# Performance work log

Hardware: AMD Instinct MI355X
Metric: run time of the kernel (lower is better)

## Reference

```python
import jax, jax.numpy as jnp
import numpy as np
from functools import partial

ALPHA, TAG, L, B = 128, 64, 50, 4096
EMB, CTX, ATT, FREQ, OUTLEN = 40, 20, 100, 60, 50
START = 1  # Alphabet.start_integer


def _sinusoid(n, d):
    # RNN_Absolute_Position: standard sinusoidal positional code, d freqs
    pos = jnp.arange(n, dtype=jnp.float32)[:, None]
    i = jnp.arange(d // 2, dtype=jnp.float32)[None, :]
    ang = pos / jnp.power(10000.0, 2.0 * i / d)
    return jnp.concatenate([jnp.sin(ang), jnp.cos(ang)], axis=-1)  # [n, d]


def _shift_back(x, k):   # value at t-k (zeros for t<k); OffsetWindows(-k)
    return jnp.pad(x, ((k, 0), (0, 0), (0, 0)))[: x.shape[0]]


def _shift_fwd(x, k):    # value at t+k (zeros past end); OffsetWindows(+k)
    return jnp.pad(x, ((0, k), (0, 0), (0, 0)))[k:]


def setup_inputs() -> dict:
    key = jax.random.key(0)
    ks = jax.random.split(key, 16)

    def lin(k, din, dout):
        k1, k2 = jax.random.split(k)
        s = 1.0 / np.sqrt(din)
        return (jax.random.uniform(k1, (din, dout), minval=-s, maxval=s),
                jax.random.uniform(k2, (dout,), minval=-s, maxval=s))

    W_ce, b_ce = lin(ks[0], EMB, CTX)                      # encoder context_embedder
    W_b4, b_b4 = lin(ks[1], 2 * CTX, CTX)                  # before_context (2 prev steps)
    W_aft, b_aft = lin(ks[2], CTX, CTX)                    # after_context (1 next step)
    W_all, b_all = lin(ks[3], 2 * CTX, CTX)                # all_context
    W_re, b_re = lin(ks[4], ALPHA, CTX)                    # decoder context_reembedder
    W_bc, b_bc = lin(ks[5], CTX, CTX)                      # decoder before_context (1 prev)
    W_q, b_q = lin(ks[6], FREQ + CTX + ALPHA + TAG, ATT)   # attention query net
    W_k, b_k = lin(ks[7], FREQ + CTX + EMB, ATT)           # attention key net
    ff_in = (CTX + EMB) + (CTX + ALPHA) + (CTX + ALPHA + TAG)
    W_ff, b_ff = lin(ks[8], ff_in, ALPHA)                  # decoder ff
    emb_table = jax.random.normal(ks[9], (ALPHA, EMB))
    lemma = jax.random.randint(ks[10], (L, B), 0, ALPHA)
    tags = jax.random.uniform(ks[11], (B, TAG))
    return dict(lemma=lemma, tags=tags, emb_table=emb_table,
                W_ce=W_ce, b_ce=b_ce, W_b4=W_b4, b_b4=b_b4,
                W_aft=W_aft, b_aft=b_aft, W_all=W_all, b_all=b_all,
                W_re=W_re, b_re=b_re, W_bc=W_bc, b_bc=b_bc,
                W_q=W_q, b_q=b_q, W_k=W_k, b_k=b_k, W_ff=W_ff, b_ff=b_ff)


def reference(lemma, tags, emb_table, W_ce, b_ce, W_b4, b_b4, W_aft, b_aft,
              W_all, b_all, W_re, b_re, W_bc, b_bc, W_q, b_q, W_k, b_k,
              W_ff, b_ff):
    Lc, Bc = lemma.shape
    sig = jax.nn.sigmoid

    # ---- LetterContextEncoder ----
    emb = emb_table[lemma]                                  # [L,B,EMB]
    ce = emb @ W_ce + b_ce                                  # [L,B,CTX]
    b4 = sig(jnp.concatenate([_shift_back(ce, 2), _shift_back(ce, 1)], -1) @ W_b4 + b_b4)
    aft = sig(_shift_fwd(ce, 1) @ W_aft + b_aft)
    ctxt = sig(jnp.concatenate([b4, aft], -1) @ W_all + b_all)  # [L,B,CTX]

    # ---- DumberDecoder (vectorized over batch) ----
    input_stack = jnp.concatenate([ctxt, emb], -1)          # [L,B,CTX+EMB]
    abs_pos = _sinusoid(OUTLEN, FREQ)                       # [OUTLEN,FREQ]
    pos_b = jnp.broadcast_to(abs_pos[:Lc, None, :], (Lc, Bc, FREQ))
    pos_stack = jnp.concatenate([pos_b, input_stack], -1)   # [L,B,120]
    K = sig(pos_stack @ W_k + b_k)                          # [L,B,ATT] precomputed keys
    V = input_stack

    # probs[0] is one-hot start token
    probs0 = jnp.zeros((Bc, ALPHA)).at[:, START].set(1.0)
    r0 = jnp.zeros((Bc, CTX))                               # reembed of probs[-1] == 0
    zeros_oa = jnp.zeros((Bc, CTX + ALPHA))                 # output_attention_results
    T = min(OUTLEN, Lc)

    def step(carry, i):
        probs_prev, r_pp = carry                            # probs[i-1], reembed(probs[i-2])
        ctx = sig(r_pp @ W_bc + b_bc)                       # output_context[i-1]
        pos_i = jnp.broadcast_to(abs_pos[i][None, :], (Bc, FREQ))
        q_in = jnp.concatenate([pos_i, ctx, probs_prev, tags], -1)
        q = sig(q_in @ W_q + b_q)                           # [B,ATT]
        scores = jnp.einsum('ba,lba->bl', q, K)
        attn = jax.nn.softmax(scores, axis=-1)
        in_attn = jnp.einsum('bl,lbd->bd', attn, V)         # [B,CTX+EMB]
        x = jnp.concatenate([in_attn, zeros_oa, ctx, probs_prev, tags], -1)
        p = jax.nn.softmax(sig(x @ W_ff + b_ff), axis=-1)   # [B,ALPHA]
        r_new = sig(probs_prev @ W_re + b_re)
        return (p, r_new), p

    _, ps = jax.lax.scan(step, (probs0, r0), jnp.arange(1, T))
    return jnp.concatenate([probs0[None], ps], axis=0)      # [T,B,ALPHA]
```

## Files before the change

### kernel.cpp

```cpp
#include <hip/hip_runtime.h>

using fp16 = _Float16;
typedef fp16 f16x4 __attribute__((ext_vector_type(4)));
typedef fp16 f16x8 __attribute__((ext_vector_type(8)));
typedef float f32x4 __attribute__((ext_vector_type(4)));

#define DEVI __device__ __forceinline__

constexpr int LL = 50;
constexpr int BB = 4096;
constexpr int ALPHA = 128;
constexpr int CTX = 20;
constexpr int ATT = 100;
constexpr int EPB = 16;

constexpr int FQ_OFF  = 0;
constexpr int FF_OFF  = 17920;
constexpr int FR_OFF  = 46592;
constexpr int FB_OFF  = 50688;
constexpr int FTQ_OFF = 51712;
constexpr int FTF_OFF = 58880;
constexpr int FRAG_TOT= 67072;

constexpr size_t WS_FRAG = 0;
constexpr size_t WS_PQ   = 134144;
constexpr size_t WS_PK   = 156544;
constexpr size_t WS_TBL  = 178944;
constexpr int    TBL_CE  = 0;
constexpr int    TBL_EM  = 2560;
constexpr int    TBL_WK  = 7680;
constexpr int    TBL_N   = 15744;
constexpr size_t WS_K    = 210432;
constexpr size_t WS_V    = WS_K + (size_t)BB*5200*2;

constexpr int XQS = 168, XFS = 232, QBS = 104, SCS = 136, TQS = 104, ATS = 56;
constexpr int OFF_XQ = 0;
constexpr int OFF_XF = 5376;
constexpr int OFF_RP = 12800;
constexpr int OFF_QB = 14080;
constexpr int OFF_SC = 17408;
constexpr int OFF_AT = 21760;
constexpr int OFF_TQ = 23552;
constexpr int OFF_TF = 26880;
constexpr int OFF_CX = 30976;
constexpr int OFF_BB = 31616;
constexpr int OFF_V  = 31776;
constexpr int SM_TOT = 131616;

DEVI float rcpf(float x) { return __builtin_amdgcn_rcpf(x); }
DEVI float sigm(float x) { return rcpf(1.0f + __expf(-x)); }

DEVI f32x4 mfma16(f16x8 a, f16x8 b, f32x4 c) {
  return __builtin_amdgcn_mfma_f32_16x16x32_f16(a, b, c, 0, 0, 0);
}
DEVI float dot8f(f16x8 a, f16x8 b, float acc) {
  acc = __builtin_amdgcn_fdot2(__builtin_shufflevector(a,a,0,1), __builtin_shufflevector(b,b,0,1), acc, false);
  acc = __builtin_amdgcn_fdot2(__builtin_shufflevector(a,a,2,3), __builtin_shufflevector(b,b,2,3), acc, false);
  acc = __builtin_amdgcn_fdot2(__builtin_shufflevector(a,a,4,5), __builtin_shufflevector(b,b,4,5), acc, false);
  acc = __builtin_amdgcn_fdot2(__builtin_shufflevector(a,a,6,7), __builtin_shufflevector(b,b,6,7), acc, false);
  return acc;
}
DEVI float dot4f(f16x4 a, f16x4 b, float acc) {
  acc = __builtin_amdgcn_fdot2(__builtin_shufflevector(a,a,0,1), __builtin_shufflevector(b,b,0,1), acc, false);
  acc = __builtin_amdgcn_fdot2(__builtin_shufflevector(a,a,2,3), __builtin_shufflevector(b,b,2,3), acc, false);
  return acc;
}

#define DPP_STEP(OP, CTRL)                                                        \
  { int t_ = __builtin_amdgcn_update_dpp(0, __builtin_bit_cast(int, v), CTRL, 0xF, 0xF, true); \
    v = OP(v, __builtin_bit_cast(float, t_)); }
DEVI float addf(float a, float b) { return a + b; }
DEVI float redmax64(float v) {
  DPP_STEP(fmaxf, 0x111) DPP_STEP(fmaxf, 0x112) DPP_STEP(fmaxf, 0x114)
  DPP_STEP(fmaxf, 0x118) DPP_STEP(fmaxf, 0x142) DPP_STEP(fmaxf, 0x143)
  return __builtin_bit_cast(float, __builtin_amdgcn_readlane(__builtin_bit_cast(int, v), 63));
}
DEVI float redsum64(float v) {
  DPP_STEP(addf, 0x111) DPP_STEP(addf, 0x112) DPP_STEP(addf, 0x114)
  DPP_STEP(addf, 0x118) DPP_STEP(addf, 0x142) DPP_STEP(addf, 0x143)
  return __builtin_bit_cast(float, __builtin_amdgcn_readlane(__builtin_bit_cast(int, v), 63));
}

DEVI void lbar() { asm volatile("s_waitcnt lgkmcnt(0)\ns_barrier" ::: "memory"); }

__global__ void dt_setup(const float* __restrict__ embT, const float* __restrict__ Wce,
                         const float* __restrict__ bce,
                         const float* __restrict__ Wq, const float* __restrict__ bq,
                         const float* __restrict__ Wk, const float* __restrict__ bk,
                         const float* __restrict__ Wff, const float* __restrict__ Wre,
                         const float* __restrict__ Wbc, char* __restrict__ ws) {
  __shared__ float ap[LL*60];
  const int tid = threadIdx.x, bid = blockIdx.x;
  if (bid <= 1) {
    for (int i = tid; i < LL*30; i += 256) {
      int p = i / 30, k = i % 30;
      float freq = powf(10000.f, 2.0f*(float)k/60.0f);
      float ang = (float)p / freq;
      ap[p*60 + k]      = sinf(ang);
      ap[p*60 + 30 + k] = cosf(ang);
    }
    __syncthreads();
    const float* W = (bid == 0) ? Wq : Wk;
    const float* bi = (bid == 0) ? bq : bk;
    float* dst = (float*)(ws + (bid == 0 ? WS_PQ : WS_PK));
    for (int i = tid; i < LL*112; i += 256) {
      int r = i / 112, j = i % 112;
      float a = 0.f;
      if (j < ATT) {
        a = bi[j];
        for (int f = 0; f < 60; ++f) a += ap[r*60 + f]*W[f*ATT + j];
      }
      dst[i] = a;
    }
  } else if (bid == 2) {
    fp16* tbl = (fp16*)(ws + WS_TBL);
    for (int i = tid; i < ALPHA*CTX; i += 256) {
      int r = i / CTX, o = i % CTX;
      float a = bce[o];
      for (int e = 0; e < 40; ++e) a += embT[r*40 + e]*Wce[e*CTX + o];
      tbl[TBL_CE + i] = (fp16)a;
    }
    for (int i = tid; i < ALPHA*40; i += 256) tbl[TBL_EM + i] = (fp16)embT[i];
  } else if (bid == 3) {
    fp16* tbl = (fp16*)(ws + WS_TBL);
    for (int i = tid; i < 112*72; i += 256) {
      int a = i / 72, c = i % 72;
      float v = 0.f;
      if (a < ATT) {
        if (c < 20)      v = Wk[(60 + c)*ATT + a];
        else if (c < 60) v = Wk[(80 + (c-20))*ATT + a];
      }
      tbl[TBL_WK + i] = (fp16)v;
    }
  } else {
    fp16* pw = (fp16*)(ws + WS_FRAG);
    for (int gi = (bid-4)*256 + tid; gi < FRAG_TOT; gi += 28*256) {
      int t = gi, img, base, KT;
      if      (t < FF_OFF)  { img = 0; base = t - FQ_OFF;  KT = 5; }
      else if (t < FR_OFF)  { img = 1; base = t - FF_OFF;  KT = 7; }
      else if (t < FB_OFF)  { img = 2; base = t - FR_OFF;  KT = 4; }
      else if (t < FTQ_OFF) { img = 3; base = t - FB_OFF;  KT = 1; }
      else if (t < FTF_OFF) { img = 4; base = t - FTQ_OFF; KT = 2; }
      else                  { img = 5; base = t - FTF_OFF; KT = 2; }
      int j = base & 7, lane = (base >> 3) & 63, frag = base >> 9;
      int nt = frag / KT, kt = frag % KT;
      int k = kt*32 + ((lane >> 4) << 3) + j;
      int n = nt*16 + (lane & 15);
      float v = 0.f;
      if (img == 0) {
        if (n < ATT) {
          if (k < 128)      v = Wq[(80 + k)*ATT + n];
          else if (k < 148) v = Wq[(60 + (k - 128))*ATT + n];
        }
      } else if (img == 1) {
        if (k < 128)      v = Wff[(228 + k)*ALPHA + n];
        else if (k < 188) v = Wff[(k - 128)*ALPHA + n];
        else if (k < 208) v = Wff[(208 + (k - 188))*ALPHA + n];
      } else if (img == 2) {
        if (k < 128 && n < CTX) v = Wre[k*CTX + n];
      } else if (img == 3) {
        if (k < CTX && n < CTX) v = Wbc[k*CTX + n];
      } else if (img == 4) {
        if (n < ATT && k < 64)  v = Wq[(208 + k)*ATT + n];
      } else {
        if (k < 64)             v = Wff[(356 + k)*ALPHA + n];
      }
      pw[gi] = (fp16)v;
    }
  }
}

__global__ void dt_encode(const int* __restrict__ lemma,
    const float* __restrict__ Wb4, const float* __restrict__ bb4,
    const float* __restrict__ Waft, const float* __restrict__ baft,
    const float* __restrict__ Wall, const float* __restrict__ ball,
    char* __restrict__ ws) {
  __shared__ fp16 wkl[112*72];
  __shared__ float wb4[800], wa[400], wl[800];
  __shared__ float cel[LL*CTX], b4l[LL*CTX], afl[LL*CTX];
  __shared__ fp16 xin[LL*72];
  __shared__ float bi4[CTX], biA[CTX], biL[CTX];
  __shared__ int lem[52];
  const int b = blockIdx.x, tid = threadIdx.x;
  const fp16* ceg = (const fp16*)(ws + WS_TBL) + TBL_CE;
  const fp16* emg = (const fp16*)(ws + WS_TBL) + TBL_EM;

  { const uint4* s = (const uint4*)((const fp16*)(ws + WS_TBL) + TBL_WK);
    uint4* d = (uint4*)wkl;
    for (int i = tid; i < 112*72*2/16; i += 256) d[i] = s[i]; }
  { const float4* s = (const float4*)Wb4; float4* d = (float4*)wb4;
    for (int i = tid; i < 200; i += 256) d[i] = s[i]; }
  { const float4* s = (const float4*)Waft; float4* d = (float4*)wa;
    for (int i = tid; i < 100; i += 256) d[i] = s[i]; }
  { const float4* s = (const float4*)Wall; float4* d = (float4*)wl;
    for (int i = tid; i < 200; i += 256) d[i] = s[i]; }
  if (tid < CTX) { bi4[tid] = bb4[tid]; biA[tid] = baft[tid]; biL[tid] = ball[tid]; }
  if (tid < LL) lem[tid] = lemma[tid*BB + b];
  __syncthreads();

  for (int i = tid; i < LL*CTX; i += 256)
    cel[i] = (float)ceg[lem[i/CTX]*CTX + (i % CTX)];
  __syncthreads();

  for (int i = tid; i < LL*CTX; i += 256) {
    int l = i / CTX, o = i % CTX;
    float a = bi4[o];
    for (int c = 0; c < CTX; ++c) {
      float c2 = (l >= 2) ? cel[(l-2)*CTX + c] : 0.f;
      float c1 = (l >= 1) ? cel[(l-1)*CTX + c] : 0.f;
      a += c2*wb4[c*CTX + o] + c1*wb4[(CTX+c)*CTX + o];
    }
    b4l[i] = sigm(a);
    float af = biA[o];
    if (l < LL-1)
      for (int c = 0; c < CTX; ++c) af += cel[(l+1)*CTX + c]*wa[c*CTX + o];
    afl[i] = sigm(af);
  }
  __syncthreads();

  for (int i = tid; i < LL*CTX; i += 256) {
    int l = i / CTX, o = i % CTX;
    float a = biL[o];
    for (int c = 0; c < CTX; ++c)
      a += b4l[l*CTX + c]*wl[c*CTX + o] + afl[l*CTX + c]*wl[(CTX+c)*CTX + o];
    xin[l*72 + o] = (fp16)sigm(a);
  }
  for (int i = tid; i < LL*40; i += 256) {
    int l = i / 40, d = i % 40;
    xin[l*72 + 20 + d] = emg[lem[l]*40 + d];
  }
  for (int i = tid; i < LL*12; i += 256) {
    int l = i / 12, c = i % 12;
    xin[l*72 + 60 + c] = (fp16)0.f;
  }
  __syncthreads();

  const float* pkg = (const float*)(ws + WS_PK);
  fp16* Kw = (fp16*)(ws + WS_K) + (size_t)b*5200;
  for (int i = tid; i < 5200; i += 256) {
    int l = i / 104, a = i % 104;
    fp16 v = (fp16)0.f;
    if (a < ATT) {
      float acc = pkg[l*112 + a];
      const fp16* x = xin + l*72;
      const fp16* wv = wkl + a*72;
      #pragma unroll
      for (int k = 0; k < 9; ++k)
        acc = dot8f(*(const f16x8*)(x + 8*k), *(const f16x8*)(wv + 8*k), acc);
      v = (fp16)sigm(acc);
    }
    Kw[i] = v;
  }
  fp16* Vw = (fp16*)(ws + WS_V) + (size_t)b*3120;
  for (int i = tid; i < 3120; i += 256) {
    int d = i / 52, l = i % 52;
    Vw[i] = (l < LL) ? xin[l*72 + d] : (fp16)0.f;
  }
}

__global__ __launch_bounds__(1024)
void dt_decoder(const char* __restrict__ ws, const float* __restrict__ tags,
                const float* __restrict__ b_re, const float* __restrict__ b_bc,
                const float* __restrict__ bff, float* __restrict__ out) {
  extern __shared__ char sm[];
  fp16* xq   = (fp16*)(sm + OFF_XQ);
  fp16* xf   = (fp16*)(sm + OFF_XF);
  fp16* rp   = (fp16*)(sm + OFF_RP);
  fp16* qb   = (fp16*)(sm + OFF_QB);
  fp16* sc   = (fp16*)(sm + OFF_SC);
  fp16* atb  = (fp16*)(sm + OFF_AT);
  fp16* tagq = (fp16*)(sm + OFF_TQ);
  fp16* tagf = (fp16*)(sm + OFF_TF);
  fp16* ctxs = (fp16*)(sm + OFF_CX);
  float* bbv = (float*)(sm + OFF_BB);
  fp16* Vl   = (fp16*)(sm + OFF_V);
  fp16* tagsl = (fp16*)(sm + OFF_QB);

  const int tid = threadIdx.x, lane = tid & 63, w = tid >> 6;
  const int quad = lane >> 4, col = lane & 15;
  const int koff = quad * 8, r0 = quad * 4;
  const int b0 = blockIdx.x * EPB;
  const int b = b0 + w;

  { uint* z = (uint*)sm;
    for (int j = tid; j < OFF_TQ/4; j += 1024) z[j] = 0; }
  { const uint4* s = (const uint4*)(ws + WS_V + (size_t)b0*6240);
    uint4* d = (uint4*)Vl;
    for (int j = tid; j < EPB*390; j += 1024) d[j] = s[j]; }
  if (tid < CTX) { bbv[tid] = b_re[tid]; bbv[20 + tid] = b_bc[tid]; }
  const float bffr = bff[((w & 7) << 4) + col];
  __syncthreads();

  { int e = tid >> 6, c = tid & 63;
    tagsl[e*72 + c] = (fp16)tags[(size_t)(b0 + e)*64 + c]; }
  if (tid < EPB) { xq[tid*XQS + 1] = (fp16)1.f; xf[tid*XFS + 1] = (fp16)1.f; }
  if (tid < EPB*CTX) {
    int r = tid / CTX, o = tid % CTX;
    float c1 = sigm(b_bc[o]);
    xq[r*XQS + 128 + o] = (fp16)c1;
    xf[r*XFS + 188 + o] = (fp16)c1;
  }
  for (int j = tid; j < EPB*128; j += 1024) {
    int e = j >> 7, o = j & 127;
    out[(size_t)(b0 + e)*ALPHA + o] = (o == 1) ? 1.f : 0.f;
  }
  __syncthreads();

  const fp16* fw = (const fp16*)(ws + WS_FRAG);
  {
    f16x8 a0 = *(const f16x8*)(tagsl + (lane & 15)*72 + koff);
    f16x8 a1 = *(const f16x8*)(tagsl + (lane & 15)*72 + 32 + koff);
    if (w < 7) {
      f16x8 t0 = *(const f16x8*)(fw + FTQ_OFF + (((w*2 + 0) << 6) + lane)*8);
      f16x8 t1 = *(const f16x8*)(fw + FTQ_OFF + (((w*2 + 1) << 6) + lane)*8);
      f32x4 c = {0.f,0.f,0.f,0.f};
      c = mfma16(a0, t0, c); c = mfma16(a1, t1, c);
      const int colg = w*16 + col;
      if (colg < 104) {
        #pragma unroll
        for (int r = 0; r < 4; ++r) tagq[(r0 + r)*TQS + colg] = (fp16)c[r];
      }
    } else if (w >= 8) {
      f16x8 u0 = *(const f16x8*)(fw + FTF_OFF + ((((w-8)*2 + 0) << 6) + lane)*8);
      f16x8 u1 = *(const f16x8*)(fw + FTF_OFF + ((((w-8)*2 + 1) << 6) + lane)*8);
      f32x4 d = {0.f,0.f,0.f,0.f};
      d = mfma16(a0, u0, d); d = mfma16(a1, u1, d);
      const int colg = (w-8)*16 + col;
      #pragma unroll
      for (int r = 0; r < 4; ++r) tagf[(r0 + r)*128 + colg] = (fp16)(d[r] + bffr);
    }
  }

  f16x8 KW[13], wW[10];
  { const int lrow = (lane < LL) ? lane : LL-1;
    const fp16* kg = (const fp16*)(ws + WS_K) + (size_t)b*5200 + lrow*104;
    #pragma unroll
    for (int j = 0; j < 13; ++j) KW[j] = *(const f16x8*)(kg + 8*j); }
  if (w < 7) {
    #pragma unroll
    for (int kt = 0; kt < 5; ++kt)
      wW[kt] = *(const f16x8*)(fw + FQ_OFF + (((w*5 + kt) << 6) + lane)*8);
  } else if (w == 7) {
    #pragma unroll
    for (int j = 0; j < 8; ++j)
      wW[j] = *(const f16x8*)(fw + FR_OFF + ((j << 6) + lane)*8);
    wW[8] = *(const f16x8*)(fw + FB_OFF + ((0 << 6) + lane)*8);
    wW[9] = *(const f16x8*)(fw + FB_OFF + ((1 << 6) + lane)*8);
  } else {
    #pragma unroll
    for (int kt = 0; kt < 7; ++kt)
      wW[kt] = *(const f16x8*)(fw + FF_OFF + ((((w-8)*7 + kt) << 6) + lane)*8);
  }

  const float* posqg = (const float*)(ws + WS_PQ);
  const fp16* xq_a = xq + (lane & 15)*XQS + koff;
  const fp16* xf_a = xf + (lane & 15)*XFS + koff;
  const fp16* rp_a = rp + (lane & 15)*40 + koff;

  __syncthreads();

  float pA = 0.f, pB = 0.f;

  for (int i = 1; i < LL; ++i) {
    if (i > 1) {
      size_t ob = ((size_t)(i-1)*BB + b)*ALPHA;
      out[ob + lane] = pA; out[ob + 64 + lane] = pB;
    }
    if (w < 7) {
      const int colg = w*16 + col;
      float pos = posqg[i*112 + colg];
      f32x4 c0 = {0.f,0.f,0.f,0.f}, c1 = {0.f,0.f,0.f,0.f};
      c0 = mfma16(*(const f16x8*)(xq_a + 0*32), wW[0], c0);
      c1 = mfma16(*(const f16x8*)(xq_a + 1*32), wW[1], c1);
      c0 = mfma16(*(const f16x8*)(xq_a + 2*32), wW[2], c0);
      c1 = mfma16(*(const f16x8*)(xq_a + 3*32), wW[3], c1);
      c0 = mfma16(*(const f16x8*)(xq_a + 4*32), wW[4], c0);
      if (colg < 104) {
        #pragma unroll
        for (int r = 0; r < 4; ++r)
          qb[(r0 + r)*QBS + colg] =
            (fp16)sigm(c0[r] + c1[r] + pos + (float)tagq[(r0 + r)*TQS + colg]);
      }
    } else if (w == 7) {
      f32x4 c0 = {0.f,0.f,0.f,0.f}, c1 = {0.f,0.f,0.f,0.f};
      #pragma unroll
      for (int kt = 0; kt < 4; ++kt) {
        f16x8 a = *(const f16x8*)(xq_a + kt*32);
        c0 = mfma16(a, wW[kt],     c0);
        c1 = mfma16(a, wW[4 + kt], c1);
      }
      const int cA = col, cB = 16 + col;
      #pragma unroll
      for (int r = 0; r < 4; ++r) {
        rp[(r0 + r)*40 + cA] = (fp16)sigm(c0[r] + bbv[cA]);
        if (cB < CTX) rp[(r0 + r)*40 + cB] = (fp16)sigm(c1[r] + bbv[cB]);
      }
      f16x8 ar = *(const f16x8*)rp_a;
      f32x4 d0 = mfma16(ar, wW[8], (f32x4){0.f,0.f,0.f,0.f});
      f32x4 d1 = mfma16(ar, wW[9], (f32x4){0.f,0.f,0.f,0.f});
      #pragma unroll
      for (int r = 0; r < 4; ++r) {
        ctxs[(r0 + r)*20 + cA] = (fp16)sigm(d0[r] + bbv[20 + cA]);
        if (cB < CTX) ctxs[(r0 + r)*20 + cB] = (fp16)sigm(d1[r] + bbv[20 + cB]);
      }
    }
    lbar();

    {
      const fp16* qrow = qb + w*QBS;
      float a0 = 0.f, a1 = 0.f;
      #pragma unroll
      for (int k = 0; k < 12; k += 2) {
        a0 = dot8f(*(const f16x8*)(qrow + 8*k),     KW[k],   a0);
        a1 = dot8f(*(const f16x8*)(qrow + 8*(k+1)), KW[k+1], a1);
      }
      a0 = dot8f(*(const f16x8*)(qrow + 96), KW[12], a0);
      float s = (lane < LL) ? (a0 + a1) : 0.f;
      float m  = redmax64(s);
      float e  = (lane < LL) ? __expf(s - m) : 0.f;
      float su = redsum64(e);
      if (lane < LL) atb[w*ATS + lane] = (fp16)(e * rcpf(su));
      const fp16* ar = atb + w*ATS;
      const fp16* vr = Vl + (w*60 + ((lane < 60) ? lane : 59))*52;
      float v0 = 0.f, v1 = 0.f;
      #pragma unroll
      for (int k = 0; k < 12; k += 2) {
        v0 = dot4f(*(const f16x4*)(ar + 4*k),     *(const f16x4*)(vr + 4*k),     v0);
        v1 = dot4f(*(const f16x4*)(ar + 4*(k+1)), *(const f16x4*)(vr + 4*(k+1)), v1);
      }
      v0 = dot4f(*(const f16x4*)(ar + 48), *(const f16x4*)(vr + 48), v0);
      if (lane < 60) xf[w*XFS + 128 + lane] = (fp16)(v0 + v1);
    }
    lbar();

    if (w >= 8) {
      const int colg = (w-8)*16 + col;
      f32x4 c0 = {0.f,0.f,0.f,0.f}, c1 = {0.f,0.f,0.f,0.f};
      c0 = mfma16(*(const f16x8*)(xf_a + 0*32), wW[0], c0);
      c1 = mfma16(*(const f16x8*)(xf_a + 1*32), wW[1], c1);
      c0 = mfma16(*(const f16x8*)(xf_a + 2*32), wW[2], c0);
      c1 = mfma16(*(const f16x8*)(xf_a + 3*32), wW[3], c1);
      c0 = mfma16(*(const f16x8*)(xf_a + 4*32), wW[4], c0);
      c1 = mfma16(*(const f16x8*)(xf_a + 5*32), wW[5], c1);
      c0 = mfma16(*(const f16x8*)(xf_a + 6*32), wW[6], c0);
      #pragma unroll
      for (int r = 0; r < 4; ++r)
        sc[(r0 + r)*SCS + colg] =
          (fp16)sigm(c0[r] + c1[r] + (float)tagf[(r0 + r)*128 + colg]);
    }
    lbar();

    {
      float v0 = (float)sc[w*SCS + lane], v1 = (float)sc[w*SCS + 64 + lane];
      float m = redmax64(fmaxf(v0, v1));
      float e0 = __expf(v0 - m), e1 = __expf(v1 - m);
      float su = redsum64(e0 + e1);
      float inv = rcpf(su);
      pA = e0 * inv; pB = e1 * inv;
      xq[w*XQS + lane] = (fp16)pA; xq[w*XQS + 64 + lane] = (fp16)pB;
      xf[w*XFS + lane] = (fp16)pA; xf[w*XFS + 64 + lane] = (fp16)pB;
    }
    if (w == 7) {
      int r = lane & 15, cg = (lane >> 4) * 5;
      #pragma unroll
      for (int j = 0; j < 5; ++j) {
        fp16 t = ctxs[r*20 + cg + j];
        xq[r*XQS + 128 + cg + j] = t;
        xf[r*XFS + 188 + cg + j] = t;
      }
    }
    lbar();
  }
  { size_t ob = ((size_t)(LL-1)*BB + b)*ALPHA;
    out[ob + lane] = pA; out[ob + 64 + lane] = pB; }
}

extern "C" void kernel_launch(void* const* d_in, const int* in_sizes, int n_in,
                              void* d_out, int out_size, void* d_ws, size_t ws_size,
                              hipStream_t stream) {
  (void)in_sizes; (void)n_in; (void)out_size; (void)ws_size;
  const int*   lemma = (const int*)  d_in[0];
  const float* tags  = (const float*)d_in[1];
  const float* embT  = (const float*)d_in[2];
  const float* Wce   = (const float*)d_in[3];
  const float* bce   = (const float*)d_in[4];
  const float* Wb4   = (const float*)d_in[5];
  const float* bb4   = (const float*)d_in[6];
  const float* Waft  = (const float*)d_in[7];
  const float* baft  = (const float*)d_in[8];
  const float* Wall  = (const float*)d_in[9];
  const float* ball  = (const float*)d_in[10];
  const float* Wre   = (const float*)d_in[11];
  const float* bre   = (const float*)d_in[12];
  const float* Wbc   = (const float*)d_in[13];
  const float* bbc   = (const float*)d_in[14];
  const float* Wq    = (const float*)d_in[15];
  const float* bq    = (const float*)d_in[16];
  const float* Wk    = (const float*)d_in[17];
  const float* bk    = (const float*)d_in[18];
  const float* Wff   = (const float*)d_in[19];
  const float* bff   = (const float*)d_in[20];
  char* ws = (char*)d_ws;
  float* out = (float*)d_out;

  hipFuncSetAttribute((const void*)dt_decoder,
                      hipFuncAttributeMaxDynamicSharedMemorySize, SM_TOT);

  dt_setup<<<32, 256, 0, stream>>>(embT, Wce, bce, Wq, bq, Wk, bk, Wff, Wre, Wbc, ws);
  dt_encode<<<BB, 256, 0, stream>>>(lemma, Wb4, bb4, Waft, baft, Wall, ball, ws);
  dt_decoder<<<BB/EPB, 1024, SM_TOT, stream>>>(ws, tags, bre, bbc, bff, out);
}
```

Before: 522.0 us.

## Compute attention scores with MFMA and reload weight fragments per step

The per-warp attention score dot products (fdot2 over K rows held in registers) become 16x16x32 MFMA tiles. Each warp holds key fragments for 16-position chunks, and the diagonal entry for its own batch row is extracted through a new shared scratch buffer, with a small dot-product tail for the last 4 attention dims. The per-warp weight fragments (wW) are no longer held in registers. They are reloaded from global/L2 inside every step, which frees registers at the cost of repeated loads. The MFMA computes all 16x16 batch-by-position products but only the diagonal row is used, so most of that work is wasted.

```diff
diff --git a/kernel.cpp b/kernel.cpp
--- a/kernel.cpp
+++ b/kernel.cpp
@@ -34,18 +34,19 @@
 constexpr size_t WS_V    = WS_K + (size_t)BB*5200*2;
 
 constexpr int XQS = 168, XFS = 232, QBS = 104, SCS = 136, TQS = 104, ATS = 56;
-constexpr int OFF_XQ = 0;
-constexpr int OFF_XF = 5376;
-constexpr int OFF_RP = 12800;
-constexpr int OFF_QB = 14080;
-constexpr int OFF_SC = 17408;
-constexpr int OFF_AT = 21760;
-constexpr int OFF_TQ = 23552;
-constexpr int OFF_TF = 26880;
-constexpr int OFF_CX = 30976;
-constexpr int OFF_BB = 31616;
-constexpr int OFF_V  = 31776;
-constexpr int SM_TOT = 131616;
+constexpr int OFF_XQ  = 0;
+constexpr int OFF_XF  = 5376;
+constexpr int OFF_RP  = 12800;
+constexpr int OFF_QB  = 14080;
+constexpr int OFF_SC  = 17408;
+constexpr int OFF_AT  = 21760;
+constexpr int OFF_TQ  = 23552;
+constexpr int OFF_TF  = 26880;
+constexpr int OFF_CX  = 30976;
+constexpr int OFF_BB  = 31616;
+constexpr int OFF_SCW = 31776;
+constexpr int OFF_V   = 35872;
+constexpr int SM_TOT  = 135712;
 
 DEVI float rcpf(float x) { return __builtin_amdgcn_rcpf(x); }
 DEVI float sigm(float x) { return rcpf(1.0f + __expf(-x)); }
@@ -273,6 +274,7 @@
   fp16* tagf = (fp16*)(sm + OFF_TF);
   fp16* ctxs = (fp16*)(sm + OFF_CX);
   float* bbv = (float*)(sm + OFF_BB);
+  float* scw = (float*)(sm + OFF_SCW);
   fp16* Vl   = (fp16*)(sm + OFF_V);
   fp16* tagsl = (fp16*)(sm + OFF_QB);
 
@@ -288,7 +290,6 @@
     uint4* d = (uint4*)Vl;
     for (int j = tid; j < EPB*390; j += 1024) d[j] = s[j]; }
   if (tid < CTX) { bbv[tid] = b_re[tid]; bbv[20 + tid] = b_bc[tid]; }
-  const float bffr = bff[((w & 7) << 4) + col];
   __syncthreads();
 
   { int e = tid >> 6, c = tid & 63;
@@ -308,8 +309,8 @@
 
   const fp16* fw = (const fp16*)(ws + WS_FRAG);
   {
-    f16x8 a0 = *(const f16x8*)(tagsl + (lane & 15)*72 + koff);
-    f16x8 a1 = *(const f16x8*)(tagsl + (lane & 15)*72 + 32 + koff);
+    f16x8 a0 = *(const f16x8*)(tagsl + col*72 + koff);
+    f16x8 a1 = *(const f16x8*)(tagsl + col*72 + 32 + koff);
     if (w < 7) {
       f16x8 t0 = *(const f16x8*)(fw + FTQ_OFF + (((w*2 + 0) << 6) + lane)*8);
       f16x8 t1 = *(const f16x8*)(fw + FTQ_OFF + (((w*2 + 1) << 6) + lane)*8);
@@ -321,6 +322,7 @@
         for (int r = 0; r < 4; ++r) tagq[(r0 + r)*TQS + colg] = (fp16)c[r];
       }
     } else if (w >= 8) {
+      const float bffr = bff[(w-8)*16 + col];
       f16x8 u0 = *(const f16x8*)(fw + FTF_OFF + ((((w-8)*2 + 0) << 6) + lane)*8);
       f16x8 u1 = *(const f16x8*)(fw + FTF_OFF + ((((w-8)*2 + 1) << 6) + lane)*8);
       f32x4 d = {0.f,0.f,0.f,0.f};
@@ -331,31 +333,25 @@
     }
   }
 
-  f16x8 KW[13], wW[10];
-  { const int lrow = (lane < LL) ? lane : LL-1;
-    const fp16* kg = (const fp16*)(ws + WS_K) + (size_t)b*5200 + lrow*104;
+  f16x8 KF[12];
+  f16x4 ktail;
+  { const fp16* kg = (const fp16*)(ws + WS_K) + (size_t)b*5200;
     #pragma unroll
-    for (int j = 0; j < 13; ++j) KW[j] = *(const f16x8*)(kg + 8*j); }
-  if (w < 7) {
-    #pragma unroll
-    for (int kt = 0; kt < 5; ++kt)
-      wW[kt] = *(const f16x8*)(fw + FQ_OFF + (((w*5 + kt) << 6) + lane)*8);
-  } else if (w == 7) {
-    #pragma unroll
-    for (int j = 0; j < 8; ++j)
-      wW[j] = *(const f16x8*)(fw + FR_OFF + ((j << 6) + lane)*8);
-    wW[8] = *(const f16x8*)(fw + FB_OFF + ((0 << 6) + lane)*8);
-    wW[9] = *(const f16x8*)(fw + FB_OFF + ((1 << 6) + lane)*8);
-  } else {
-    #pragma unroll
-    for (int kt = 0; kt < 7; ++kt)
-      wW[kt] = *(const f16x8*)(fw + FF_OFF + ((((w-8)*7 + kt) << 6) + lane)*8);
+    for (int c = 0; c < 3; ++c) {
+      #pragma unroll
+      for (int t = 0; t < 4; ++t) {
+        int pos = t*16 + col; if (pos >= LL) pos = LL-1;
+        KF[c*4 + t] = *(const f16x8*)(kg + pos*104 + c*32 + koff);
+      }
+    }
+    int pl = (lane < LL) ? lane : LL-1;
+    ktail = *(const f16x4*)(kg + pl*104 + 96);
   }
 
   const float* posqg = (const float*)(ws + WS_PQ);
-  const fp16* xq_a = xq + (lane & 15)*XQS + koff;
-  const fp16* xf_a = xf + (lane & 15)*XFS + koff;
-  const fp16* rp_a = rp + (lane & 15)*40 + koff;
+  const fp16* xq_a = xq + col*XQS + koff;
+  const fp16* xf_a = xf + col*XFS + koff;
+  const fp16* rp_a = rp + col*40 + koff;
 
   __syncthreads();
 
@@ -369,12 +365,17 @@
     if (w < 7) {
       const int colg = w*16 + col;
       float pos = posqg[i*112 + colg];
+      f16x8 q0 = *(const f16x8*)(fw + FQ_OFF + (((w*5 + 0) << 6) + lane)*8);
+      f16x8 q1 = *(const f16x8*)(fw + FQ_OFF + (((w*5 + 1) << 6) + lane)*8);
+      f16x8 q2 = *(const f16x8*)(fw + FQ_OFF + (((w*5 + 2) << 6) + lane)*8);
+      f16x8 q3 = *(const f16x8*)(fw + FQ_OFF + (((w*5 + 3) << 6) + lane)*8);
+      f16x8 q4 = *(const f16x8*)(fw + FQ_OFF + (((w*5 + 4) << 6) + lane)*8);
       f32x4 c0 = {0.f,0.f,0.f,0.f}, c1 = {0.f,0.f,0.f,0.f};
-      c0 = mfma16(*(const f16x8*)(xq_a + 0*32), wW[0], c0);
-      c1 = mfma16(*(const f16x8*)(xq_a + 1*32), wW[1], c1);
-      c0 = mfma16(*(const f16x8*)(xq_a + 2*32), wW[2], c0);
-      c1 = mfma16(*(const f16x8*)(xq_a + 3*32), wW[3], c1);
-      c0 = mfma16(*(const f16x8*)(xq_a + 4*32), wW[4], c0);
+      c0 = mfma16(*(const f16x8*)(xq_a + 0*32), q0, c0);
+      c1 = mfma16(*(const f16x8*)(xq_a + 1*32), q1, c1);
+      c0 = mfma16(*(const f16x8*)(xq_a + 2*32), q2, c0);
+      c1 = mfma16(*(const f16x8*)(xq_a + 3*32), q3, c1);
+      c0 = mfma16(*(const f16x8*)(xq_a + 4*32), q4, c0);
       if (colg < 104) {
         #pragma unroll
         for (int r = 0; r < 4; ++r)
@@ -385,9 +386,11 @@
       f32x4 c0 = {0.f,0.f,0.f,0.f}, c1 = {0.f,0.f,0.f,0.f};
       #pragma unroll
       for (int kt = 0; kt < 4; ++kt) {
+        f16x8 w0 = *(const f16x8*)(fw + FR_OFF + (((0*4 + kt) << 6) + lane)*8);
+        f16x8 w1 = *(const f16x8*)(fw + FR_OFF + (((1*4 + kt) << 6) + lane)*8);
         f16x8 a = *(const f16x8*)(xq_a + kt*32);
-        c0 = mfma16(a, wW[kt],     c0);
-        c1 = mfma16(a, wW[4 + kt], c1);
+        c0 = mfma16(a, w0, c0);
+        c1 = mfma16(a, w1, c1);
       }
       const int cA = col, cB = 16 + col;
       #pragma unroll
@@ -395,9 +398,11 @@
         rp[(r0 + r)*40 + cA] = (fp16)sigm(c0[r] + bbv[cA]);
         if (cB < CTX) rp[(r0 + r)*40 + cB] = (fp16)sigm(c1[r] + bbv[cB]);
       }
+      f16x8 wb0 = *(const f16x8*)(fw + FB_OFF + ((0 << 6) + lane)*8);
+      f16x8 wb1 = *(const f16x8*)(fw + FB_OFF + ((1 << 6) + lane)*8);
       f16x8 ar = *(const f16x8*)rp_a;
-      f32x4 d0 = mfma16(ar, wW[8], (f32x4){0.f,0.f,0.f,0.f});
-      f32x4 d1 = mfma16(ar, wW[9], (f32x4){0.f,0.f,0.f,0.f});
+      f32x4 d0 = mfma16(ar, wb0, (f32x4){0.f,0.f,0.f,0.f});
+      f32x4 d1 = mfma16(ar, wb1, (f32x4){0.f,0.f,0.f,0.f});
       #pragma unroll
       for (int r = 0; r < 4; ++r) {
         ctxs[(r0 + r)*20 + cA] = (fp16)sigm(d0[r] + bbv[20 + cA]);
@@ -407,15 +412,27 @@
     lbar();
 
     {
-      const fp16* qrow = qb + w*QBS;
-      float a0 = 0.f, a1 = 0.f;
-      #pragma unroll
-      for (int k = 0; k < 12; k += 2) {
-        a0 = dot8f(*(const f16x8*)(qrow + 8*k),     KW[k],   a0);
-        a1 = dot8f(*(const f16x8*)(qrow + 8*(k+1)), KW[k+1], a1);
-      }
-      a0 = dot8f(*(const f16x8*)(qrow + 96), KW[12], a0);
-      float s = (lane < LL) ? (a0 + a1) : 0.f;
+      f32x4 s0 = {0.f,0.f,0.f,0.f}, s1 = {0.f,0.f,0.f,0.f};
+      f32x4 s2 = {0.f,0.f,0.f,0.f}, s3 = {0.f,0.f,0.f,0.f};
+      #pragma unroll
+      for (int c = 0; c < 3; ++c) {
+        f16x8 a = *(const f16x8*)(qb + col*QBS + c*32 + koff);
+        s0 = mfma16(a, KF[c*4 + 0], s0);
+        s1 = mfma16(a, KF[c*4 + 1], s1);
+        s2 = mfma16(a, KF[c*4 + 2], s2);
+        s3 = mfma16(a, KF[c*4 + 3], s3);
+      }
+      if (quad == (w >> 2)) {
+        const int sel = w & 3;
+        float* sw = scw + w*64;
+        sw[ 0 + col] = sel==0 ? s0[0] : sel==1 ? s0[1] : sel==2 ? s0[2] : s0[3];
+        sw[16 + col] = sel==0 ? s1[0] : sel==1 ? s1[1] : sel==2 ? s1[2] : s1[3];
+        sw[32 + col] = sel==0 ? s2[0] : sel==1 ? s2[1] : sel==2 ? s2[2] : s2[3];
+        sw[48 + col] = sel==0 ? s3[0] : sel==1 ? s3[1] : sel==2 ? s3[2] : s3[3];
+      }
+      f16x4 qt = *(const f16x4*)(qb + w*QBS + 96);
+      float s = scw[w*64 + lane] + dot4f(qt, ktail, 0.f);
+      s = (lane < LL) ? s : 0.f;
       float m  = redmax64(s);
       float e  = (lane < LL) ? __expf(s - m) : 0.f;
       float su = redsum64(e);
@@ -435,14 +452,21 @@
 
     if (w >= 8) {
       const int colg = (w-8)*16 + col;
+      f16x8 f0 = *(const f16x8*)(fw + FF_OFF + ((((w-8)*7 + 0) << 6) + lane)*8);
+      f16x8 f1 = *(const f16x8*)(fw + FF_OFF + ((((w-8)*7 + 1) << 6) + lane)*8);
+      f16x8 f2 = *(const f16x8*)(fw + FF_OFF + ((((w-8)*7 + 2) << 6) + lane)*8);
+      f16x8 f3 = *(const f16x8*)(fw + FF_OFF + ((((w-8)*7 + 3) << 6) + lane)*8);
+      f16x8 f4 = *(const f16x8*)(fw + FF_OFF + ((((w-8)*7 + 4) << 6) + lane)*8);
+      f16x8 f5 = *(const f16x8*)(fw + FF_OFF + ((((w-8)*7 + 5) << 6) + lane)*8);
+      f16x8 f6 = *(const f16x8*)(fw + FF_OFF + ((((w-8)*7 + 6) << 6) + lane)*8);
       f32x4 c0 = {0.f,0.f,0.f,0.f}, c1 = {0.f,0.f,0.f,0.f};
-      c0 = mfma16(*(const f16x8*)(xf_a + 0*32), wW[0], c0);
-      c1 = mfma16(*(const f16x8*)(xf_a + 1*32), wW[1], c1);
-      c0 = mfma16(*(const f16x8*)(xf_a + 2*32), wW[2], c0);
-      c1 = mfma16(*(const f16x8*)(xf_a + 3*32), wW[3], c1);
-      c0 = mfma16(*(const f16x8*)(xf_a + 4*32), wW[4], c0);
-      c1 = mfma16(*(const f16x8*)(xf_a + 5*32), wW[5], c1);
-      c0 = mfma16(*(const f16x8*)(xf_a + 6*32), wW[6], c0);
+      c0 = mfma16(*(const f16x8*)(xf_a + 0*32), f0, c0);
+      c1 = mfma16(*(const f16x8*)(xf_a + 1*32), f1, c1);
+      c0 = mfma16(*(const f16x8*)(xf_a + 2*32), f2, c0);
+      c1 = mfma16(*(const f16x8*)(xf_a + 3*32), f3, c1);
+      c0 = mfma16(*(const f16x8*)(xf_a + 4*32), f4, c0);
+      c1 = mfma16(*(const f16x8*)(xf_a + 5*32), f5, c1);
+      c0 = mfma16(*(const f16x8*)(xf_a + 6*32), f6, c0);
       #pragma unroll
       for (int r = 0; r < 4; ++r)
         sc[(r0 + r)*SCS + colg] =
```

Result: faster. 498.4 us (median of 3 runs) (-4.5%).
